# Kernel tuning notes

Hardware: AMD Instinct MI355X
Metric: run time of the kernel (lower is better)

## Reference

```python
import jax, jax.numpy as jnp
import numpy as np

# Module constants (from init_kwargs)
K_BUDGET = 16      # selector budget K
R_REFRAC = 1       # refractory separation r
LAM = 0.5          # selector regularization lambda
MAX_PROXY = 64     # max_proxy_points (K_eff cap)


def setup_inputs() -> dict:
    key = jax.random.key(0)
    ks = jax.random.split(key, 8)
    B, T, D = 32, 4096, 128
    H, K_LIFT, D_MODEL = 256, 64, 1024
    g = lambda i, shape, s=0.05: jax.random.normal(ks[i], shape, jnp.float32) * s
    return {
        "x": jax.random.normal(ks[0], (B, T, D), jnp.float32),
        "W1": g(1, (D, H)),
        "b1": jnp.zeros((H,), jnp.float32),
        "w_e": g(2, (H,)),
        "w_s": g(3, (H,)),
        "W_lift": g(4, (D + 3, K_LIFT)),
        "b_lift": jnp.zeros((K_LIFT,), jnp.float32),
        "W_proj": g(5, (K_LIFT, D_MODEL)),
        "b_proj": jnp.zeros((D_MODEL,), jnp.float32),
        "log_temperature": jnp.zeros((), jnp.float32),
    }


def _soft_selector(saliency, log_temperature):
    """SoftSelectorProxy.forward: sigmoid relaxation of budget+refractory QP."""
    T = saliency.shape[1]
    temp = jnp.clip(jnp.exp(log_temperature), 0.1, 10.0)
    logits = (saliency / (2.0 * LAM) - 0.5) / temp
    y = jax.nn.sigmoid(logits)
    y = y.at[:, 0].set(0.0)
    budget = jnp.clip(y.sum(axis=1, keepdims=True), 1e-6)
    y = y * jnp.minimum(K_BUDGET / budget, 1.0)
    for d in range(1, min(R_REFRAC + 1, T)):  # r=1 -> single unrolled step
        pair_sum = y + jnp.roll(y, -d, axis=1)
        y = y * jnp.minimum(2.0 / (1.0 + pair_sum), 1.0)
    y = y.at[:, 0].set(0.0)
    return y


def reference(x, W1, b1, w_e, w_s, W_lift, b_lift, W_proj, b_proj, log_temperature):
    B, T, D = x.shape
    # 1. CausalEventModel: per-step MLP -> event scores + saliency  [B,T]
    h = jnp.tanh(jnp.einsum("btd,dh->bth", x, W1) + b1)
    event_scores = h @ w_e                       # [B,T] (unused downstream)
    saliency = jax.nn.softplus(h @ w_s)          # [B,T], nonnegative saliency
    # 2. Relaxed selector proxy -> continuous anchor weights y*  [B,T]
    y_star = _soft_selector(saliency, log_temperature)
    # 3. Dense anchor vectors: x augmented with 3 topology features (anchor_dim = D+3)
    tpos = jnp.broadcast_to(jnp.arange(T, dtype=x.dtype) / T, (B, T))
    cums = jnp.cumsum(saliency, axis=1)
    dense = jnp.concatenate(
        [x, saliency[..., None], tpos[..., None], cums[..., None]], axis=-1
    )  # [B,T,D+3]
    # 4. NormalizedLift: linear lift to k dims, L2-normalized cloud  [B,T,k]
    lifted = jnp.einsum("bta,ak->btk", dense, W_lift) + b_lift
    lifted = lifted / jnp.clip(
        jnp.linalg.norm(lifted, axis=-1, keepdims=True), 1e-6
    )
    # 5. Top-K anchor selection + gather + projection  [B,K_eff,d_model]
    K_eff = min(T, MAX_PROXY)
    _, top_idx = jax.lax.top_k(y_star, K_eff)                 # [B,K_eff]
    cloud = jnp.take_along_axis(lifted, top_idx[..., None], axis=1)  # [B,K_eff,k]
    tokens = jnp.einsum("bnk,kd->bnd", cloud, W_proj) + b_proj
    return tokens, y_star
```

## Files before the change

### kernel.cpp

```cpp
#include <hip/hip_runtime.h>
#include <math.h>

#define TT 4096
#define BB 32
#define DD 128
#define HH 256
#define KL 64
#define DM 1024
#define KEFF 64
#define KBUDGET 16.0f
#define LAM_ 0.5f

__device__ __forceinline__ float fast_tanh(float x) {
#if __has_builtin(__builtin_amdgcn_exp2f)
  float e = __builtin_amdgcn_exp2f(x * 2.885390081777927f);
#else
  float e = __expf(2.0f * x);
#endif
  float r = __builtin_amdgcn_rcpf(e + 1.0f);
  return fmaf(-2.0f, r, 1.0f);
}

__global__ __launch_bounds__(256, 2) void k_sal(const float* __restrict__ x,
    const float* __restrict__ W1, const float* __restrict__ b1,
    const float* __restrict__ w_s, float* __restrict__ sal_out)
{
  __shared__ float xs[64][132];
  __shared__ float redsm[4][64];

  const int tid  = threadIdx.x;
  const int lane = tid & 63;
  const int wave = tid >> 6;
  const int rq = lane & 7;
  const int hq = lane >> 3;
  const int h0 = wave * 64 + hq * 8;
  const long rowbase = (long)blockIdx.x * 64;

  #pragma unroll
  for (int p = 0; p < 8; ++p) {
    int i = tid + p * 256;
    int r = i >> 5, c4 = i & 31;
    float4 v = *(const float4*)&x[(rowbase + r) * DD + c4 * 4];
    *(float4*)&xs[r][c4 * 4] = v;
  }
  __syncthreads();

  float acc[8][8];
  #pragma unroll
  for (int i = 0; i < 8; ++i)
    #pragma unroll
    for (int j = 0; j < 8; ++j) acc[i][j] = 0.f;

  const float* __restrict__ Wb = W1 + h0;

#define LOADW(BUF, D4)                                        \
  {                                                           \
    const float* wp = Wb + (size_t)(D4) * 4 * HH;             \
    BUF[0] = *(const float4*)&wp[0];                          \
    BUF[1] = *(const float4*)&wp[4];                          \
    BUF[2] = *(const float4*)&wp[HH];                         \
    BUF[3] = *(const float4*)&wp[HH + 4];                     \
    BUF[4] = *(const float4*)&wp[2 * HH];                     \
    BUF[5] = *(const float4*)&wp[2 * HH + 4];                 \
    BUF[6] = *(const float4*)&wp[3 * HH];                     \
    BUF[7] = *(const float4*)&wp[3 * HH + 4];                 \
  }

#define FMAROW(I, XD, WA, WB)                      \
  acc[I][0] = fmaf(XD, WA.x, acc[I][0]);           \
  acc[I][1] = fmaf(XD, WA.y, acc[I][1]);           \
  acc[I][2] = fmaf(XD, WA.z, acc[I][2]);           \
  acc[I][3] = fmaf(XD, WA.w, acc[I][3]);           \
  acc[I][4] = fmaf(XD, WB.x, acc[I][4]);           \
  acc[I][5] = fmaf(XD, WB.y, acc[I][5]);           \
  acc[I][6] = fmaf(XD, WB.z, acc[I][6]);           \
  acc[I][7] = fmaf(XD, WB.w, acc[I][7]);
#define FMAD(C, WA, WB)                            \
  FMAROW(0, xv0.C, WA, WB)                         \
  FMAROW(1, xv1.C, WA, WB)                         \
  FMAROW(2, xv2.C, WA, WB)                         \
  FMAROW(3, xv3.C, WA, WB)                         \
  FMAROW(4, xv4.C, WA, WB)                         \
  FMAROW(5, xv5.C, WA, WB)                         \
  FMAROW(6, xv6.C, WA, WB)                         \
  FMAROW(7, xv7.C, WA, WB)

#define FMABLOCK(D4, W)                                       \
  {                                                           \
    float4 xv0 = *(const float4*)&xs[rq +  0][(D4) * 4];      \
    float4 xv1 = *(const float4*)&xs[rq +  8][(D4) * 4];      \
    float4 xv2 = *(const float4*)&xs[rq + 16][(D4) * 4];      \
    float4 xv3 = *(const float4*)&xs[rq + 24][(D4) * 4];      \
    float4 xv4 = *(const float4*)&xs[rq + 32][(D4) * 4];      \
    float4 xv5 = *(const float4*)&xs[rq + 40][(D4) * 4];      \
    float4 xv6 = *(const float4*)&xs[rq + 48][(D4) * 4];      \
    float4 xv7 = *(const float4*)&xs[rq + 56][(D4) * 4];      \
    FMAD(x, W[0], W[1])                                       \
    FMAD(y, W[2], W[3])                                       \
    FMAD(z, W[4], W[5])                                       \
    FMAD(w, W[6], W[7])                                       \
  }

  float4 wA[8], wB[8];
  LOADW(wA, 0)
  #pragma unroll 1
  for (int d4 = 0; d4 < 30; d4 += 2) {
    LOADW(wB, d4 + 1)
    FMABLOCK(d4, wA)
    LOADW(wA, d4 + 2)
    FMABLOCK(d4 + 1, wB)
  }
  LOADW(wB, 31)
  FMABLOCK(30, wA)
  FMABLOCK(31, wB)

#undef FMABLOCK
#undef FMAD
#undef FMAROW
#undef LOADW

  float4 ba  = *(const float4*)&b1[h0];
  float4 bb  = *(const float4*)&b1[h0 + 4];
  float4 wsa = *(const float4*)&w_s[h0];
  float4 wsb = *(const float4*)&w_s[h0 + 4];
  float s_acc[8];
  #pragma unroll
  for (int i = 0; i < 8; ++i) {
    float s = 0.f;
    s = fmaf(fast_tanh(acc[i][0] + ba.x), wsa.x, s);
    s = fmaf(fast_tanh(acc[i][1] + ba.y), wsa.y, s);
    s = fmaf(fast_tanh(acc[i][2] + ba.z), wsa.z, s);
    s = fmaf(fast_tanh(acc[i][3] + ba.w), wsa.w, s);
    s = fmaf(fast_tanh(acc[i][4] + bb.x), wsb.x, s);
    s = fmaf(fast_tanh(acc[i][5] + bb.y), wsb.y, s);
    s = fmaf(fast_tanh(acc[i][6] + bb.z), wsb.z, s);
    s = fmaf(fast_tanh(acc[i][7] + bb.w), wsb.w, s);
    s_acc[i] = s;
  }
  #pragma unroll
  for (int m = 8; m < 64; m <<= 1) {
    #pragma unroll
    for (int i = 0; i < 8; ++i) s_acc[i] += __shfl_xor(s_acc[i], m, 64);
  }
  if (hq == 0) {
    #pragma unroll
    for (int i = 0; i < 8; ++i) redsm[wave][rq + 8 * i] = s_acc[i];
  }
  __syncthreads();
  if (tid < 64) {
    float z = redsm[0][tid] + redsm[1][tid] + redsm[2][tid] + redsm[3][tid];
    float sp = fmaxf(z, 0.f) + log1pf(expf(-fabsf(z)));
    sal_out[rowbase + tid] = sp;
  }
}

__global__ __launch_bounds__(256) void k_sel(const float* __restrict__ logt,
    float* __restrict__ ysr, int* __restrict__ topidx,
    float* __restrict__ topsal, float* __restrict__ topcums)
{
  __shared__ float sal[TT];
  __shared__ float ya[TT];
  __shared__ float yb[TT];
  __shared__ float redf[8];
  __shared__ float wl_val[4][KEFF];
  __shared__ int   wl_idx[4][KEFF];

  const int tid = threadIdx.x;
  const int lane = tid & 63;
  const int wave = tid >> 6;
  const int b = blockIdx.x;
  float* row = ysr + (long)b * TT;

  for (int i = tid; i < TT; i += 256) sal[i] = row[i];
  __syncthreads();

  float temp = expf(logt[0]);
  temp = fminf(fmaxf(temp, 0.1f), 10.f);
  const float inv2lam = 1.0f / (2.0f * LAM_);

  for (int i = tid; i < TT; i += 256) {
    float z = (sal[i] * inv2lam - 0.5f) / temp;
    float s;
    if (z >= 0.f) { float e = expf(-z); s = 1.f / (1.f + e); }
    else          { float e = expf(z);  s = e / (1.f + e); }
    ya[i] = (i == 0) ? 0.f : s;
  }
  __syncthreads();

  float loc = 0.f;
  for (int i = tid; i < TT; i += 256) loc += ya[i];
  #pragma unroll
  for (int m = 1; m < 64; m <<= 1) loc += __shfl_xor(loc, m, 64);
  if (lane == 0) redf[wave] = loc;
  __syncthreads();
  float budget = redf[0] + redf[1] + redf[2] + redf[3];
  float scale = fminf(KBUDGET / fmaxf(budget, 1e-6f), 1.f);

  for (int i = tid; i < TT; i += 256) {
    float yi = ya[i] * scale;
    float yj = ya[(i + 1) & (TT - 1)] * scale;
    float m = fminf(2.f / (1.f + (yi + yj)), 1.f);
    yb[i] = (i == 0) ? 0.f : yi * m;
  }
  __syncthreads();

  for (int i = tid; i < TT; i += 256) row[i] = yb[i];

  const int base = tid * 16;
  float run = 0.f;
  #pragma unroll
  for (int j = 0; j < 16; ++j) { run += sal[base + j]; ya[base + j] = run; }
  float v = run;
  #pragma unroll
  for (int m = 1; m < 64; m <<= 1) {
    float u = __shfl_up(v, (unsigned)m, 64);
    if (lane >= m) v += u;
  }
  float lexcl = v - run;
  if (lane == 63) redf[4 + wave] = v;
  __syncthreads();
  float woff = 0.f;
  for (int w = 0; w < wave; ++w) woff += redf[4 + w];
  float off = woff + lexcl;
  #pragma unroll
  for (int j = 0; j < 16; ++j) ya[base + j] += off;
  __syncthreads();

  const int qb = wave * 1024 + lane * 16;
  float lv[16];
  #pragma unroll
  for (int j = 0; j < 16; ++j) lv[j] = yb[qb + j];
  unsigned rm = 0;
  float bv = -1.f; int bi = 1 << 30;
  #pragma unroll
  for (int j = 0; j < 16; ++j)
    if (lv[j] > bv) { bv = lv[j]; bi = qb + j; }

  for (int it = 0; it < KEFF; ++it) {
    float cv = bv; int ci = bi;
    #pragma unroll
    for (int m = 1; m < 64; m <<= 1) {
      float ov = __shfl_xor(cv, m, 64);
      int   oi = __shfl_xor(ci, m, 64);
      if (ov > cv || (ov == cv && oi < ci)) { cv = ov; ci = oi; }
    }
    if (lane == 0) { wl_val[wave][it] = cv; wl_idx[wave][it] = ci; }
    if (ci >= qb && ci < qb + 16) {
      rm |= 1u << (ci - qb);
      bv = -1.f; bi = 1 << 30;
      #pragma unroll
      for (int j = 0; j < 16; ++j)
        if (!((rm >> j) & 1u) && lv[j] > bv) { bv = lv[j]; bi = qb + j; }
    }
  }
  __syncthreads();

  if (tid == 0) {
    int p0 = 0, p1 = 0, p2 = 0, p3 = 0;
    float v0 = wl_val[0][0], v1 = wl_val[1][0], v2 = wl_val[2][0], v3 = wl_val[3][0];
    int   i0 = wl_idx[0][0], i1 = wl_idx[1][0], i2 = wl_idx[2][0], i3 = wl_idx[3][0];
    for (int it = 0; it < KEFF; ++it) {
      float va = v0; int ia = i0; int sa = 0;
      if (v1 > va || (v1 == va && i1 < ia)) { va = v1; ia = i1; sa = 1; }
      if (v2 > va || (v2 == va && i2 < ia)) { va = v2; ia = i2; sa = 2; }
      if (v3 > va || (v3 == va && i3 < ia)) { va = v3; ia = i3; sa = 3; }
      topidx[b * KEFF + it]  = ia;
      topsal[b * KEFF + it]  = sal[ia];
      topcums[b * KEFF + it] = ya[ia];
      if      (sa == 0) { ++p0; v0 = (p0 < KEFF) ? wl_val[0][p0] : -1.f; i0 = (p0 < KEFF) ? wl_idx[0][p0] : (1 << 30); }
      else if (sa == 1) { ++p1; v1 = (p1 < KEFF) ? wl_val[1][p1] : -1.f; i1 = (p1 < KEFF) ? wl_idx[1][p1] : (1 << 30); }
      else if (sa == 2) { ++p2; v2 = (p2 < KEFF) ? wl_val[2][p2] : -1.f; i2 = (p2 < KEFF) ? wl_idx[2][p2] : (1 << 30); }
      else              { ++p3; v3 = (p3 < KEFF) ? wl_val[3][p3] : -1.f; i3 = (p3 < KEFF) ? wl_idx[3][p3] : (1 << 30); }
    }
  }
}

__global__ __launch_bounds__(256) void k_tok(const float* __restrict__ x,
    const float* __restrict__ W_lift, const float* __restrict__ b_lift,
    const float* __restrict__ W_proj, const float* __restrict__ b_proj,
    const int* __restrict__ topidx, const float* __restrict__ topsal,
    const float* __restrict__ topcums, float* __restrict__ tokens)
{
  __shared__ float cloud[8][KL];
  const int tid = threadIdx.x;
  const int k = tid & 63;
  const int g = tid >> 6;
  const int b = blockIdx.x >> 3;
  const int nb = (blockIdx.x & 7) * 8;

  #pragma unroll
  for (int a = 0; a < 2; ++a) {
    int n = nb + g + a * 4;
    int t = topidx[b * KEFF + n];
    const float* xr = x + ((long)b * TT + t) * DD;
    float acc = 0.f;
    #pragma unroll 8
    for (int d4 = 0; d4 < DD / 4; ++d4) {
      float4 xv = *(const float4*)&xr[d4 * 4];
      acc = fmaf(xv.x, W_lift[(d4 * 4 + 0) * KL + k], acc);
      acc = fmaf(xv.y, W_lift[(d4 * 4 + 1) * KL + k], acc);
      acc = fmaf(xv.z, W_lift[(d4 * 4 + 2) * KL + k], acc);
      acc = fmaf(xv.w, W_lift[(d4 * 4 + 3) * KL + k], acc);
    }
    float s  = topsal[b * KEFF + n];
    float tp = (float)t / (float)TT;
    float cm = topcums[b * KEFF + n];
    acc = fmaf(s,  W_lift[128 * KL + k], acc);
    acc = fmaf(tp, W_lift[129 * KL + k], acc);
    acc = fmaf(cm, W_lift[130 * KL + k], acc);
    acc += b_lift[k];
    float ss = acc * acc;
    #pragma unroll
    for (int m = 1; m < 64; m <<= 1) ss += __shfl_xor(ss, m, 64);
    float denom = fmaxf(sqrtf(ss), 1e-6f);
    cloud[g + a * 4][k] = acc / denom;
  }
  __syncthreads();

  #pragma unroll
  for (int q = 0; q < 4; ++q) {
    int dcol = tid + q * 256;
    float accp[8];
    #pragma unroll
    for (int n = 0; n < 8; ++n) accp[n] = 0.f;
    for (int kk = 0; kk < KL; ++kk) {
      float w = W_proj[kk * DM + dcol];
      #pragma unroll
      for (int n = 0; n < 8; ++n) accp[n] = fmaf(cloud[n][kk], w, accp[n]);
    }
    float bp = b_proj[dcol];
    #pragma unroll
    for (int n = 0; n < 8; ++n)
      tokens[((long)b * KEFF + nb + n) * DM + dcol] = accp[n] + bp;
  }
}

extern "C" void kernel_launch(void* const* d_in, const int* in_sizes, int n_in,
                              void* d_out, int out_size, void* d_ws, size_t ws_size,
                              hipStream_t stream) {
  const float* x      = (const float*)d_in[0];
  const float* W1     = (const float*)d_in[1];
  const float* b1     = (const float*)d_in[2];
  const float* w_s    = (const float*)d_in[4];
  const float* W_lift = (const float*)d_in[5];
  const float* b_lift = (const float*)d_in[6];
  const float* W_proj = (const float*)d_in[7];
  const float* b_proj = (const float*)d_in[8];
  const float* logt   = (const float*)d_in[9];

  float* tokens = (float*)d_out;
  float* ysr    = tokens + (size_t)BB * KEFF * DM;
  int*   topidx  = (int*)d_ws;
  float* topsal  = (float*)((char*)d_ws + 8192);
  float* topcums = (float*)((char*)d_ws + 16384);

  k_sal<<<(BB * TT) / 64, 256, 0, stream>>>(x, W1, b1, w_s, ysr);
  k_sel<<<BB, 256, 0, stream>>>(logt, ysr, topidx, topsal, topcums);
  k_tok<<<BB * 8, 256, 0, stream>>>(x, W_lift, b_lift, W_proj, b_proj,
                                    topidx, topsal, topcums, tokens);
}
```

Baseline: 235.5 us.

## Make saliency kernel persistent over four tiles with double-buffered x prefetch

Each k_sal block now processes four 64-row tiles instead of one, so the grid shrinks from 2048 to 512 blocks. While one tile is computed, the next tile's x is prefetched into registers and then written to a second LDS buffer, hiding global load latency behind the FMA loop. Bias and w_s loads are hoisted out of the tile loop. In exchange, LDS use doubles, register pressure rises from the 8 held float4 prefetch values, and there are fewer blocks to spread across the CUs, which may hurt occupancy or tail balance.

New measurement: 272.2 us. 1.16x slower.

```diff
diff --git a/kernel.cpp b/kernel.cpp
--- a/kernel.cpp
+++ b/kernel.cpp
@@ -25,7 +25,7 @@
     const float* __restrict__ W1, const float* __restrict__ b1,
     const float* __restrict__ w_s, float* __restrict__ sal_out)
 {
-  __shared__ float xs[64][132];
+  __shared__ float xs[2][64][132];
   __shared__ float redsm[4][64];
 
   const int tid  = threadIdx.x;
@@ -34,24 +34,28 @@
   const int rq = lane & 7;
   const int hq = lane >> 3;
   const int h0 = wave * 64 + hq * 8;
-  const long rowbase = (long)blockIdx.x * 64;
-
-  #pragma unroll
-  for (int p = 0; p < 8; ++p) {
-    int i = tid + p * 256;
-    int r = i >> 5, c4 = i & 31;
-    float4 v = *(const float4*)&x[(rowbase + r) * DD + c4 * 4];
-    *(float4*)&xs[r][c4 * 4] = v;
-  }
-  __syncthreads();
-
-  float acc[8][8];
-  #pragma unroll
-  for (int i = 0; i < 8; ++i)
-    #pragma unroll
-    for (int j = 0; j < 8; ++j) acc[i][j] = 0.f;
-
+  const int sr = tid >> 5;
+  const int sc = tid & 31;
+
+  const float4 ba  = *(const float4*)&b1[h0];
+  const float4 bb  = *(const float4*)&b1[h0 + 4];
+  const float4 wsa = *(const float4*)&w_s[h0];
+  const float4 wsb = *(const float4*)&w_s[h0 + 4];
   const float* __restrict__ Wb = W1 + h0;
+
+#define SLOAD(REG, TILE)                                               \
+  {                                                                    \
+    const float* xb = x + ((long)(TILE) * 64) * DD;                    \
+    _Pragma("unroll")                                                  \
+    for (int p = 0; p < 8; ++p)                                        \
+      REG[p] = *(const float4*)&xb[(sr + p * 8) * DD + sc * 4];        \
+  }
+#define SWRITE(REG, BUF)                                               \
+  {                                                                    \
+    _Pragma("unroll")                                                  \
+    for (int p = 0; p < 8; ++p)                                        \
+      *(float4*)&xs[BUF][sr + p * 8][sc * 4] = REG[p];                 \
+  }
 
 #define LOADW(BUF, D4)                                        \
   {                                                           \
@@ -87,71 +91,96 @@
 
 #define FMABLOCK(D4, W)                                       \
   {                                                           \
-    float4 xv0 = *(const float4*)&xs[rq +  0][(D4) * 4];      \
-    float4 xv1 = *(const float4*)&xs[rq +  8][(D4) * 4];      \
-    float4 xv2 = *(const float4*)&xs[rq + 16][(D4) * 4];      \
-    float4 xv3 = *(const float4*)&xs[rq + 24][(D4) * 4];      \
-    float4 xv4 = *(const float4*)&xs[rq + 32][(D4) * 4];      \
-    float4 xv5 = *(const float4*)&xs[rq + 40][(D4) * 4];      \
-    float4 xv6 = *(const float4*)&xs[rq + 48][(D4) * 4];      \
-    float4 xv7 = *(const float4*)&xs[rq + 56][(D4) * 4];      \
+    float4 xv0 = *(const float4*)&X[rq +  0][(D4) * 4];       \
+    float4 xv1 = *(const float4*)&X[rq +  8][(D4) * 4];       \
+    float4 xv2 = *(const float4*)&X[rq + 16][(D4) * 4];       \
+    float4 xv3 = *(const float4*)&X[rq + 24][(D4) * 4];       \
+    float4 xv4 = *(const float4*)&X[rq + 32][(D4) * 4];       \
+    float4 xv5 = *(const float4*)&X[rq + 40][(D4) * 4];       \
+    float4 xv6 = *(const float4*)&X[rq + 48][(D4) * 4];       \
+    float4 xv7 = *(const float4*)&X[rq + 56][(D4) * 4];       \
     FMAD(x, W[0], W[1])                                       \
     FMAD(y, W[2], W[3])                                       \
     FMAD(z, W[4], W[5])                                       \
     FMAD(w, W[6], W[7])                                       \
   }
 
-  float4 wA[8], wB[8];
-  LOADW(wA, 0)
+  const int tile0 = blockIdx.x * 4;
+  float4 xreg[8];
+
+  SLOAD(xreg, tile0)
+  SWRITE(xreg, 0)
+  __syncthreads();
+
   #pragma unroll 1
-  for (int d4 = 0; d4 < 30; d4 += 2) {
-    LOADW(wB, d4 + 1)
-    FMABLOCK(d4, wA)
-    LOADW(wA, d4 + 2)
-    FMABLOCK(d4 + 1, wB)
-  }
-  LOADW(wB, 31)
-  FMABLOCK(30, wA)
-  FMABLOCK(31, wB)
+  for (int r = 0; r < 4; ++r) {
+    const int cur = r & 1;
+    const int tile = tile0 + r;
+
+    if (r < 3) SLOAD(xreg, tile + 1)
+
+    float acc[8][8];
+    #pragma unroll
+    for (int i = 0; i < 8; ++i)
+      #pragma unroll
+      for (int j = 0; j < 8; ++j) acc[i][j] = 0.f;
+
+    const float (*__restrict__ X)[132] = xs[cur];
+
+    float4 wA[8], wB[8];
+    LOADW(wA, 0)
+    #pragma unroll 1
+    for (int d4 = 0; d4 < 30; d4 += 2) {
+      LOADW(wB, d4 + 1)
+      FMABLOCK(d4, wA)
+      LOADW(wA, d4 + 2)
+      FMABLOCK(d4 + 1, wB)
+    }
+    LOADW(wB, 31)
+    FMABLOCK(30, wA)
+    FMABLOCK(31, wB)
+
+    float s_acc[8];
+    #pragma unroll
+    for (int i = 0; i < 8; ++i) {
+      float s = 0.f;
+      s = fmaf(fast_tanh(acc[i][0] + ba.x), wsa.x, s);
+      s = fmaf(fast_tanh(acc[i][1] + ba.y), wsa.y, s);
+      s = fmaf(fast_tanh(acc[i][2] + ba.z), wsa.z, s);
+      s = fmaf(fast_tanh(acc[i][3] + ba.w), wsa.w, s);
+      s = fmaf(fast_tanh(acc[i][4] + bb.x), wsb.x, s);
+      s = fmaf(fast_tanh(acc[i][5] + bb.y), wsb.y, s);
+      s = fmaf(fast_tanh(acc[i][6] + bb.z), wsb.z, s);
+      s = fmaf(fast_tanh(acc[i][7] + bb.w), wsb.w, s);
+      s_acc[i] = s;
+    }
+    #pragma unroll
+    for (int m = 8; m < 64; m <<= 1) {
+      #pragma unroll
+      for (int i = 0; i < 8; ++i) s_acc[i] += __shfl_xor(s_acc[i], m, 64);
+    }
+    if (hq == 0) {
+      #pragma unroll
+      for (int i = 0; i < 8; ++i) redsm[wave][rq + 8 * i] = s_acc[i];
+    }
+
+    if (r < 3) SWRITE(xreg, cur ^ 1)
+    __syncthreads();
+
+    if (tid < 64) {
+      float z = redsm[0][tid] + redsm[1][tid] + redsm[2][tid] + redsm[3][tid];
+      float sp = fmaxf(z, 0.f) + log1pf(expf(-fabsf(z)));
+      sal_out[(long)tile * 64 + tid] = sp;
+    }
+    __syncthreads();
+  }
 
 #undef FMABLOCK
 #undef FMAD
 #undef FMAROW
 #undef LOADW
-
-  float4 ba  = *(const float4*)&b1[h0];
-  float4 bb  = *(const float4*)&b1[h0 + 4];
-  float4 wsa = *(const float4*)&w_s[h0];
-  float4 wsb = *(const float4*)&w_s[h0 + 4];
-  float s_acc[8];
-  #pragma unroll
-  for (int i = 0; i < 8; ++i) {
-    float s = 0.f;
-    s = fmaf(fast_tanh(acc[i][0] + ba.x), wsa.x, s);
-    s = fmaf(fast_tanh(acc[i][1] + ba.y), wsa.y, s);
-    s = fmaf(fast_tanh(acc[i][2] + ba.z), wsa.z, s);
-    s = fmaf(fast_tanh(acc[i][3] + ba.w), wsa.w, s);
-    s = fmaf(fast_tanh(acc[i][4] + bb.x), wsb.x, s);
-    s = fmaf(fast_tanh(acc[i][5] + bb.y), wsb.y, s);
-    s = fmaf(fast_tanh(acc[i][6] + bb.z), wsb.z, s);
-    s = fmaf(fast_tanh(acc[i][7] + bb.w), wsb.w, s);
-    s_acc[i] = s;
-  }
-  #pragma unroll
-  for (int m = 8; m < 64; m <<= 1) {
-    #pragma unroll
-    for (int i = 0; i < 8; ++i) s_acc[i] += __shfl_xor(s_acc[i], m, 64);
-  }
-  if (hq == 0) {
-    #pragma unroll
-    for (int i = 0; i < 8; ++i) redsm[wave][rq + 8 * i] = s_acc[i];
-  }
-  __syncthreads();
-  if (tid < 64) {
-    float z = redsm[0][tid] + redsm[1][tid] + redsm[2][tid] + redsm[3][tid];
-    float sp = fmaxf(z, 0.f) + log1pf(expf(-fabsf(z)));
-    sal_out[rowbase + tid] = sp;
-  }
+#undef SWRITE
+#undef SLOAD
 }
 
 __global__ __launch_bounds__(256) void k_sel(const float* __restrict__ logt,
@@ -354,7 +383,7 @@
   float* topsal  = (float*)((char*)d_ws + 8192);
   float* topcums = (float*)((char*)d_ws + 16384);
 
-  k_sal<<<(BB * TT) / 64, 256, 0, stream>>>(x, W1, b1, w_s, ysr);
+  k_sal<<<512, 256, 0, stream>>>(x, W1, b1, w_s, ysr);
   k_sel<<<BB, 256, 0, stream>>>(logt, ysr, topidx, topsal, topcums);
   k_tok<<<BB * 8, 256, 0, stream>>>(x, W_lift, b_lift, W_proj, b_proj,
                                     topidx, topsal, topcums, tokens);
```
